# Kernel optimization log

Hardware: AMD Instinct MI355X
Metric: run time of the kernel (lower is better)

## Reference

```python
import jax, jax.numpy as jnp
import numpy as np

N_NODES = 100000
N_EDGES = 600000
D_IN = 128
D_HID = 128
N_CLASSES = 64


def setup_inputs() -> dict:
    key = jax.random.key(0)
    ks = jax.random.split(key, 8)
    x = jax.random.normal(ks[0], (N_NODES, D_IN), dtype=jnp.float32)
    src = jax.random.randint(ks[1], (N_EDGES,), 0, N_NODES, dtype=jnp.int32)
    dst = jax.random.randint(ks[2], (N_EDGES,), 0, N_NODES, dtype=jnp.int32)
    s = 1.0 / np.sqrt(D_IN)
    W_self1 = jax.random.normal(ks[3], (D_IN, D_HID), dtype=jnp.float32) * s
    W_neigh1 = jax.random.normal(ks[4], (D_IN, D_HID), dtype=jnp.float32) * s
    b1 = jnp.zeros((D_HID,), dtype=jnp.float32)
    s2 = 1.0 / np.sqrt(D_HID)
    W_self2 = jax.random.normal(ks[5], (D_HID, N_CLASSES), dtype=jnp.float32) * s2
    W_neigh2 = jax.random.normal(ks[6], (D_HID, N_CLASSES), dtype=jnp.float32) * s2
    b2 = jnp.zeros((N_CLASSES,), dtype=jnp.float32)
    return {"x": x, "src": src, "dst": dst,
            "W_self1": W_self1, "W_neigh1": W_neigh1, "b1": b1,
            "W_self2": W_self2, "W_neigh2": W_neigh2, "b2": b2}


def _sage_conv(h, src, dst, W_self, W_neigh, b):
    # mean aggregation over in-neighbors (DGL SAGEConv 'mean')
    n = h.shape[0]
    nbr_sum = jax.ops.segment_sum(h[src], dst, num_segments=n)  # [N, d]
    deg = jax.ops.segment_sum(jnp.ones(src.shape, h.dtype), dst, num_segments=n)
    nbr_mean = nbr_sum / jnp.maximum(deg, 1.0)[:, None]
    return h @ W_self + nbr_mean @ W_neigh + b


def reference(x, src, dst, W_self1, W_neigh1, b1, W_self2, W_neigh2, b2):
    # dropout is identity in eval mode
    h = _sage_conv(x, src, dst, W_self1, W_neigh1, b1)
    h = jax.nn.relu(h)
    h = _sage_conv(h, src, dst, W_self2, W_neigh2, b2)
    return h
```

## Files before the change

### kernel.cpp

```cpp
#include <hip/hip_runtime.h>

#define N_NODES 100000
#define N_EDGES 600000
#define K_DIM 128
#define M2 64
#define NT_TILES ((N_NODES + 63) / 64)
#define GEMM_GRID 256

#define NBKT 800
#define NPB 125
#define HIST_BLOCKS 64
#define EPB (N_EDGES / HIST_BLOCKS)
#define BSTRIDE 1024

using frag_ab = __attribute__((ext_vector_type(8))) short;
using frag_cd = __attribute__((ext_vector_type(4))) float;

__device__ __forceinline__ unsigned short f2b(float f) {
  unsigned u = __builtin_bit_cast(unsigned, f);
  u = (u + 0x7fffu + ((u >> 16) & 1u)) >> 16;
  return (unsigned short)u;
}

__device__ __forceinline__ void gload_lds16(const void* gsrc, void* ldst) {
  __builtin_amdgcn_global_load_lds(
      (const __attribute__((address_space(1))) void*)gsrc,
      (__attribute__((address_space(3))) void*)ldst, 16, 0, 0);
}

__device__ __forceinline__ void lgkm_barrier() {
  __builtin_amdgcn_sched_barrier(0);
  asm volatile("s_waitcnt lgkmcnt(0)" ::: "memory");
  __builtin_amdgcn_s_barrier();
  __builtin_amdgcn_sched_barrier(0);
}

#define XB_BLOCKS ((N_NODES * K_DIM / 4 + 255) / 256)
#define W_ELEMS ((128 + 128 + 64 + 64) * 128)
#define WB_BLOCKS ((W_ELEMS + 255) / 256)
__global__ __launch_bounds__(256) void conv_all(const float* __restrict__ x,
                                                unsigned short* __restrict__ xb,
                                                const float* __restrict__ Ws1,
                                                const float* __restrict__ Wn1,
                                                const float* __restrict__ Ws2,
                                                const float* __restrict__ Wn2,
                                                unsigned short* __restrict__ Ws1T,
                                                unsigned short* __restrict__ Wn1T,
                                                unsigned short* __restrict__ Ws2T,
                                                unsigned short* __restrict__ Wn2T,
                                                const int* __restrict__ src,
                                                const int* __restrict__ dst,
                                                int* __restrict__ gbucket,
                                                int* __restrict__ ebuf) {
  __shared__ int lcnt[NBKT];
  __shared__ int lbase[NBKT];
  if (blockIdx.x < HIST_BLOCKS) {
    int tid = threadIdx.x;
    for (int i = tid; i < NBKT; i += 256) lcnt[i] = 0;
    __syncthreads();
    int e0 = blockIdx.x * EPB;
    for (int e = e0 + tid; e < e0 + EPB; e += 256)
      atomicAdd(&lcnt[dst[e] / NPB], 1);
    __syncthreads();
    for (int i = tid; i < NBKT; i += 256) {
      int c = lcnt[i];
      lbase[i] = c ? atomicAdd(&gbucket[i], c) : 0;
      lcnt[i] = 0;
    }
    __syncthreads();
    for (int e = e0 + tid; e < e0 + EPB; e += 256) {
      int d = dst[e];
      int b = d / NPB;
      int p = lbase[b] + atomicAdd(&lcnt[b], 1);
      ebuf[b * BSTRIDE + p] = src[e] | ((d - b * NPB) << 20);
    }
  } else if (blockIdx.x < HIST_BLOCKS + XB_BLOCKS) {
    long i = (long)(blockIdx.x - HIST_BLOCKS) * 256 + threadIdx.x;
    if (i >= (long)N_NODES * K_DIM / 4) return;
    float4 v = *(const float4*)(x + i * 4);
    ushort4 o;
    o.x = f2b(v.x); o.y = f2b(v.y); o.z = f2b(v.z); o.w = f2b(v.w);
    *(ushort4*)(xb + i * 4) = o;
  } else {
    int i = (blockIdx.x - HIST_BLOCKS - XB_BLOCKS) * 256 + threadIdx.x;
    if (i >= W_ELEMS) return;
    const float* W;
    unsigned short* WT;
    int M, li;
    if (i < 128 * 128)               { W = Ws1; WT = Ws1T; M = 128; li = i; }
    else if (i < 2 * 128 * 128)      { W = Wn1; WT = Wn1T; M = 128; li = i - 128 * 128; }
    else if (i < 2 * 128 * 128 + 64 * 128) { W = Ws2; WT = Ws2T; M = 64; li = i - 2 * 128 * 128; }
    else                             { W = Wn2; WT = Wn2T; M = 64; li = i - 2 * 128 * 128 - 64 * 128; }
    int n = li >> 7, k = li & 127;
    WT[li] = f2b(W[k * M + n]);
  }
}

__global__ __launch_bounds__(512) void bucket_csr_agg1(const unsigned short* __restrict__ xb,
                                                       const int* __restrict__ ebuf,
                                                       const int* __restrict__ gbucket,
                                                       int* __restrict__ rp,
                                                       int* __restrict__ csr_src,
                                                       unsigned short* __restrict__ aggb) {
  __shared__ int cnt[128];
  __shared__ int sedge[BSTRIDE];
  int tid = threadIdx.x, b = blockIdx.x;
  int bs = b * BSTRIDE;
  int ecnt = gbucket[b];
  for (int i = tid; i < 128; i += 512) cnt[i] = 0;
  __syncthreads();

  int ln[2], lp[2], sv[2];
#pragma unroll
  for (int j = 0; j < 2; ++j) {
    int p = tid + j * 512;
    if (p < ecnt) {
      int pk = ebuf[bs + p];
      sv[j] = pk & 0xFFFFF;
      ln[j] = pk >> 20;
      lp[j] = atomicAdd(&cnt[ln[j]], 1);
    }
  }
  __syncthreads();
  for (int off = 1; off < 128; off <<= 1) {
    int t = 0;
    if (tid < 128 && tid >= off) t = cnt[tid - off];
    __syncthreads();
    if (tid < 128) cnt[tid] += t;
    __syncthreads();
  }
  for (int i = tid; i < 126; i += 512)
    rp[b * 126 + i] = bs + (i ? cnt[i - 1] : 0);
#pragma unroll
  for (int j = 0; j < 2; ++j) {
    int p = tid + j * 512;
    if (p < ecnt) {
      int l = ln[j];
      int loc = (l ? cnt[l - 1] : 0) + lp[j];
      sedge[loc] = sv[j];
      csr_src[bs + loc] = sv[j];
    }
  }
  __syncthreads();

  int nl = tid >> 4;
  int c = (tid & 15) << 3;
  for (int n0 = 0; n0 < NPB; n0 += 32) {
    int node = n0 + nl;
    if (node < NPB) {
      int beg = node ? cnt[node - 1] : 0;
      int end = cnt[node];
      float acc[8];
#pragma unroll
      for (int j = 0; j < 8; ++j) acc[j] = 0.f;
      for (int e0 = beg; e0 < end; e0 += 8) {
        int idx[8];
#pragma unroll
        for (int p = 0; p < 8; ++p) idx[p] = sedge[min(e0 + p, end - 1)];
        uint4 v[8];
#pragma unroll
        for (int p = 0; p < 8; ++p) v[p] = *(const uint4*)(xb + (size_t)idx[p] * K_DIM + c);
#pragma unroll
        for (int p = 0; p < 8; ++p) {
          float m = (e0 + p < end) ? 1.f : 0.f;
          unsigned u[4] = {v[p].x, v[p].y, v[p].z, v[p].w};
#pragma unroll
          for (int j = 0; j < 4; ++j) {
            acc[2 * j]     += m * __builtin_bit_cast(float, u[j] << 16);
            acc[2 * j + 1] += m * __builtin_bit_cast(float, u[j] & 0xffff0000u);
          }
        }
      }
      float inv = 1.0f / (float)max(end - beg, 1);
      uint4 o;
      unsigned* op = (unsigned*)&o;
#pragma unroll
      for (int j = 0; j < 4; ++j) {
        unsigned lo = f2b(acc[2 * j] * inv);
        unsigned hi = f2b(acc[2 * j + 1] * inv);
        op[j] = lo | (hi << 16);
      }
      *(uint4*)(aggb + (size_t)(b * NPB + node) * K_DIM + c) = o;
    }
  }
}

__global__ __launch_bounds__(256) void aggregate64_add(const unsigned short* __restrict__ g,
                                                       const int* __restrict__ rp,
                                                       const int* __restrict__ csr_src,
                                                       float* __restrict__ out, int n) {
  int t = blockIdx.x * blockDim.x + threadIdx.x;
  int node = t >> 3;
  int c = (t & 7) << 3;
  if (node >= n) return;
  int b = node / NPB;
  int i = node - b * NPB;
  int beg = rp[b * 126 + i], end = rp[b * 126 + i + 1];
  float acc[8];
#pragma unroll
  for (int j = 0; j < 8; ++j) acc[j] = 0.f;

  if (end > beg) {
    for (int e0 = beg; e0 < end; e0 += 8) {
      int idx[8];
#pragma unroll
      for (int p = 0; p < 8; ++p) idx[p] = csr_src[min(e0 + p, end - 1)];
      uint4 v[8];
#pragma unroll
      for (int p = 0; p < 8; ++p) v[p] = *(const uint4*)(g + (size_t)idx[p] * M2 + c);
#pragma unroll
      for (int p = 0; p < 8; ++p) {
        float m = (e0 + p < end) ? 1.f : 0.f;
        unsigned u[4] = {v[p].x, v[p].y, v[p].z, v[p].w};
#pragma unroll
        for (int j = 0; j < 4; ++j) {
          acc[2 * j]     += m * __builtin_bit_cast(float, u[j] << 16);
          acc[2 * j + 1] += m * __builtin_bit_cast(float, u[j] & 0xffff0000u);
        }
      }
    }
  }
  float inv = 1.0f / (float)max(end - beg, 1);
  float* op = out + (size_t)node * M2 + c;
  float4 o0 = *(float4*)(op);
  float4 o1 = *(float4*)(op + 4);
  o0.x += acc[0] * inv; o0.y += acc[1] * inv; o0.z += acc[2] * inv; o0.w += acc[3] * inv;
  o1.x += acc[4] * inv; o1.y += acc[5] * inv; o1.z += acc[6] * inv; o1.w += acc[7] * inv;
  *(float4*)(op) = o0;
  *(float4*)(op + 4) = o1;
}

__device__ __forceinline__ void stage_tile(const unsigned short* xb, const unsigned short* aggb,
                                           int t, char* dstbase, int tid, int wave, int N) {
#pragma unroll
  for (int it = 0; it < 2; ++it) {
    int L = it * 8192 + tid * 16;
    int row = L >> 8;
    int srb = (L & 255) ^ ((row & 7) << 4);
    int node = t * 64 + row;
    if (node >= N) node = N - 1;
    char* d = dstbase + it * 8192 + wave * 1024;
    gload_lds16((const char*)xb + (size_t)node * 256 + srb, d);
    gload_lds16((const char*)aggb + (size_t)node * 256 + srb, d + 16384);
  }
}

__global__ __launch_bounds__(512, 2) void sage_fused_gemm(const unsigned short* __restrict__ xb,
                                                          const unsigned short* __restrict__ aggb,
                                                          const unsigned short* __restrict__ Ws1T,
                                                          const unsigned short* __restrict__ Wn1T,
                                                          const float* __restrict__ b1,
                                                          const unsigned short* __restrict__ Ws2T,
                                                          const unsigned short* __restrict__ Wn2T,
                                                          const float* __restrict__ b2,
                                                          float* __restrict__ out,
                                                          unsigned short* __restrict__ g, int N) {
  __shared__ char sL[163840];

  const int tid = threadIdx.x;
  const int wave = tid >> 6;
  const int lane = tid & 63;
  const int l15 = lane & 15;
  const int q = lane >> 4;
  const int nodeq = wave >> 1;
  const int fhalf = wave & 1;
  const int fbase = fhalf * 64;

#pragma unroll
  for (int it = 0; it < 4; ++it) {
    int L = it * 8192 + tid * 16;
    int row = L >> 8;
    int srb = (L & 255) ^ ((row & 7) << 4);
    char* d = sL + it * 8192 + wave * 1024;
    gload_lds16((const char*)Ws1T + row * 256 + srb, d);
    gload_lds16((const char*)Wn1T + row * 256 + srb, d + 32768);
  }
#pragma unroll
  for (int it = 0; it < 2; ++it) {
    int L = it * 8192 + tid * 16;
    int row = L >> 8;
    int srb = (L & 255) ^ ((row & 7) << 4);
    char* d = sL + 65536 + it * 8192 + wave * 1024;
    gload_lds16((const char*)Ws2T + row * 256 + srb, d);
    gload_lds16((const char*)Wn2T + row * 256 + srb, d + 16384);
  }
  int tt = blockIdx.x;
  if (tt < NT_TILES) stage_tile(xb, aggb, tt, sL + 98304, tid, wave, N);

  float4 bv1[4], bv2[4];
#pragma unroll
  for (int ft = 0; ft < 4; ++ft) {
    bv1[ft] = *(const float4*)(b1 + fbase + ft * 16 + q * 4);
    bv2[ft] = *(const float4*)(b2 + ft * 16 + q * 4);
  }

  int li = 0;
  for (; tt < NT_TILES; tt += GEMM_GRID, ++li) {
    char* cur = sL + 98304 + (li & 1) * 32768;
    char* nxt = sL + 98304 + ((li + 1) & 1) * 32768;

    __syncthreads();

    if (tt + GEMM_GRID < NT_TILES)
      stage_tile(xb, aggb, tt + GEMM_GRID, nxt, tid, wave, N);

    frag_cd acc[4];
#pragma unroll
    for (int ft = 0; ft < 4; ++ft) acc[ft] = (frag_cd)(0.f);

    const int xrow = nodeq * 16 + l15;
    const int xswz = (xrow & 7) << 4;
#pragma unroll
    for (int kb = 0; kb < 4; ++kb) {
      int base = kb * 64 + q * 16;
      frag_ab axk = *(const frag_ab*)(cur + xrow * 256 + (base ^ xswz));
      frag_ab agk = *(const frag_ab*)(cur + 16384 + xrow * 256 + (base ^ xswz));
      frag_ab fs[4], fn[4];
#pragma unroll
      for (int ft = 0; ft < 4; ++ft) {
        int wrow = fbase + ft * 16 + l15;
        int woff = base ^ ((wrow & 7) << 4);
        fs[ft] = *(const frag_ab*)(sL + wrow * 256 + woff);
        fn[ft] = *(const frag_ab*)(sL + 32768 + wrow * 256 + woff);
      }
#pragma unroll
      for (int ft = 0; ft < 4; ++ft) {
        acc[ft] = __builtin_amdgcn_mfma_f32_16x16x32_bf16(fs[ft], axk, acc[ft], 0, 0, 0);
        acc[ft] = __builtin_amdgcn_mfma_f32_16x16x32_bf16(fn[ft], agk, acc[ft], 0, 0, 0);
      }
    }

    lgkm_barrier();

#pragma unroll
    for (int ft = 0; ft < 4; ++ft) {
      int f0 = fbase + ft * 16 + q * 4;
      ushort4 o;
      o.x = f2b(fmaxf(acc[ft][0] + bv1[ft].x, 0.f));
      o.y = f2b(fmaxf(acc[ft][1] + bv1[ft].y, 0.f));
      o.z = f2b(fmaxf(acc[ft][2] + bv1[ft].z, 0.f));
      o.w = f2b(fmaxf(acc[ft][3] + bv1[ft].w, 0.f));
      *(ushort4*)(cur + xrow * 256 + ((f0 * 2) ^ xswz)) = o;
    }

    lgkm_barrier();

    const char* w2b = sL + 65536 + fhalf * 16384;
    frag_cd acc2[4];
#pragma unroll
    for (int ft = 0; ft < 4; ++ft) acc2[ft] = (frag_cd)(0.f);

#pragma unroll
    for (int kb = 0; kb < 4; ++kb) {
      int base = kb * 64 + q * 16;
      frag_ab ah = *(const frag_ab*)(cur + xrow * 256 + (base ^ xswz));
      frag_ab w2[4];
#pragma unroll
      for (int ft = 0; ft < 4; ++ft) {
        int wr = ft * 16 + l15;
        w2[ft] = *(const frag_ab*)(w2b + wr * 256 + (base ^ ((wr & 7) << 4)));
      }
#pragma unroll
      for (int ft = 0; ft < 4; ++ft)
        acc2[ft] = __builtin_amdgcn_mfma_f32_16x16x32_bf16(w2[ft], ah, acc2[ft], 0, 0, 0);
    }

    int node = tt * 64 + nodeq * 16 + l15;
    if (node < N) {
      if (fhalf == 0) {
#pragma unroll
        for (int ft = 0; ft < 4; ++ft) {
          int f0 = ft * 16 + q * 4;
          float4 o;
          o.x = acc2[ft][0] + bv2[ft].x;
          o.y = acc2[ft][1] + bv2[ft].y;
          o.z = acc2[ft][2] + bv2[ft].z;
          o.w = acc2[ft][3] + bv2[ft].w;
          *(float4*)(out + (size_t)node * M2 + f0) = o;
        }
      } else {
#pragma unroll
        for (int ft = 0; ft < 4; ++ft) {
          int f0 = ft * 16 + q * 4;
          ushort4 o;
          o.x = f2b(acc2[ft][0]);
          o.y = f2b(acc2[ft][1]);
          o.z = f2b(acc2[ft][2]);
          o.w = f2b(acc2[ft][3]);
          *(ushort4*)(g + (size_t)node * M2 + f0) = o;
        }
      }
    }
  }
}

extern "C" void kernel_launch(void* const* d_in, const int* in_sizes, int n_in,
                              void* d_out, int out_size, void* d_ws, size_t ws_size,
                              hipStream_t stream) {
  const float* x   = (const float*)d_in[0];
  const int*   src = (const int*)d_in[1];
  const int*   dst = (const int*)d_in[2];
  const float* Ws1 = (const float*)d_in[3];
  const float* Wn1 = (const float*)d_in[4];
  const float* b1  = (const float*)d_in[5];
  const float* Ws2 = (const float*)d_in[6];
  const float* Wn2 = (const float*)d_in[7];
  const float* b2  = (const float*)d_in[8];
  float* out = (float*)d_out;

  char* ws = (char*)d_ws;
  size_t off = 0;
  auto alloc = [&](size_t bytes) {
    void* p = ws + off;
    off = (off + bytes + 4095) & ~(size_t)4095;
    return p;
  };
  int* gbucket  = (int*)alloc((size_t)NBKT * 4);
  int* ebuf     = (int*)alloc((size_t)NBKT * BSTRIDE * 4);
  int* rp       = (int*)alloc((size_t)NBKT * 126 * 4);
  int* csr_src  = (int*)alloc((size_t)NBKT * BSTRIDE * 4);
  unsigned short* xb   = (unsigned short*)alloc((size_t)N_NODES * K_DIM * 2);
  unsigned short* aggb = (unsigned short*)alloc((size_t)N_NODES * K_DIM * 2);
  unsigned short* g    = (unsigned short*)alloc((size_t)N_NODES * M2 * 2);
  unsigned short* Ws1T = (unsigned short*)alloc((size_t)128 * 128 * 2);
  unsigned short* Wn1T = (unsigned short*)alloc((size_t)128 * 128 * 2);
  unsigned short* Ws2T = (unsigned short*)alloc((size_t)64 * 128 * 2);
  unsigned short* Wn2T = (unsigned short*)alloc((size_t)64 * 128 * 2);

  hipMemsetAsync(gbucket, 0, (size_t)NBKT * 4, stream);

  conv_all<<<HIST_BLOCKS + XB_BLOCKS + WB_BLOCKS, 256, 0, stream>>>(
      x, xb, Ws1, Wn1, Ws2, Wn2, Ws1T, Wn1T, Ws2T, Wn2T, src, dst, gbucket, ebuf);

  bucket_csr_agg1<<<NBKT, 512, 0, stream>>>(xb, ebuf, gbucket, rp, csr_src, aggb);

  sage_fused_gemm<<<GEMM_GRID, 512, 0, stream>>>(
      xb, aggb, Ws1T, Wn1T, b1, Ws2T, Wn2T, b2, out, g, N_NODES);

  {
    long t = (long)N_NODES * 8;
    aggregate64_add<<<(int)((t + 255) / 256), 256, 0, stream>>>(g, rp, csr_src, out, N_NODES);
  }
}
```

Baseline: 213.0 us.

## Split edge bucket scatter into a separate wide kernel with precomputed positions

After: 203.2 us. -4.6%, faster.

```diff
diff --git a/kernel.cpp b/kernel.cpp
--- a/kernel.cpp
+++ b/kernel.cpp
@@ -35,7 +35,7 @@
   __builtin_amdgcn_sched_barrier(0);
 }
 
-#define XB_BLOCKS ((N_NODES * K_DIM / 4 + 255) / 256)
+#define XB_BLOCKS ((N_NODES * K_DIM / 8 + 255) / 256)
 #define W_ELEMS ((128 + 128 + 64 + 64) * 128)
 #define WB_BLOCKS ((W_ELEMS + 255) / 256)
 __global__ __launch_bounds__(256) void conv_all(const float* __restrict__ x,
@@ -48,39 +48,39 @@
                                                 unsigned short* __restrict__ Wn1T,
                                                 unsigned short* __restrict__ Ws2T,
                                                 unsigned short* __restrict__ Wn2T,
-                                                const int* __restrict__ src,
                                                 const int* __restrict__ dst,
+                                                int* __restrict__ pos,
                                                 int* __restrict__ gbucket,
-                                                int* __restrict__ ebuf) {
+                                                int* __restrict__ base_tbl) {
   __shared__ int lcnt[NBKT];
-  __shared__ int lbase[NBKT];
   if (blockIdx.x < HIST_BLOCKS) {
     int tid = threadIdx.x;
     for (int i = tid; i < NBKT; i += 256) lcnt[i] = 0;
     __syncthreads();
     int e0 = blockIdx.x * EPB;
-    for (int e = e0 + tid; e < e0 + EPB; e += 256)
-      atomicAdd(&lcnt[dst[e] / NPB], 1);
+    for (int e = e0 + tid; e < e0 + EPB; e += 256) {
+      int b = dst[e] / NPB;
+      pos[e] = atomicAdd(&lcnt[b], 1);
+    }
     __syncthreads();
     for (int i = tid; i < NBKT; i += 256) {
       int c = lcnt[i];
-      lbase[i] = c ? atomicAdd(&gbucket[i], c) : 0;
-      lcnt[i] = 0;
-    }
-    __syncthreads();
-    for (int e = e0 + tid; e < e0 + EPB; e += 256) {
-      int d = dst[e];
-      int b = d / NPB;
-      int p = lbase[b] + atomicAdd(&lcnt[b], 1);
-      ebuf[b * BSTRIDE + p] = src[e] | ((d - b * NPB) << 20);
+      if (c) base_tbl[blockIdx.x * NBKT + i] = atomicAdd(&gbucket[i], c);
     }
   } else if (blockIdx.x < HIST_BLOCKS + XB_BLOCKS) {
-    long i = (long)(blockIdx.x - HIST_BLOCKS) * 256 + threadIdx.x;
+    long t = (long)(blockIdx.x - HIST_BLOCKS) * 256 + threadIdx.x;
+    long i = t * 2;
     if (i >= (long)N_NODES * K_DIM / 4) return;
-    float4 v = *(const float4*)(x + i * 4);
-    ushort4 o;
-    o.x = f2b(v.x); o.y = f2b(v.y); o.z = f2b(v.z); o.w = f2b(v.w);
-    *(ushort4*)(xb + i * 4) = o;
+    float4 v0 = *(const float4*)(x + i * 4);
+    float4 v1 = *(const float4*)(x + i * 4 + 4);
+    ushort4 o0, o1;
+    o0.x = f2b(v0.x); o0.y = f2b(v0.y); o0.z = f2b(v0.z); o0.w = f2b(v0.w);
+    o1.x = f2b(v1.x); o1.y = f2b(v1.y); o1.z = f2b(v1.z); o1.w = f2b(v1.w);
+    *(uint4*)(xb + i * 4) = uint4{
+        (unsigned)o0.x | ((unsigned)o0.y << 16),
+        (unsigned)o0.z | ((unsigned)o0.w << 16),
+        (unsigned)o1.x | ((unsigned)o1.y << 16),
+        (unsigned)o1.z | ((unsigned)o1.w << 16)};
   } else {
     int i = (blockIdx.x - HIST_BLOCKS - XB_BLOCKS) * 256 + threadIdx.x;
     if (i >= W_ELEMS) return;
@@ -94,6 +94,19 @@
     int n = li >> 7, k = li & 127;
     WT[li] = f2b(W[k * M + n]);
   }
+}
+
+__global__ __launch_bounds__(256) void bucket_scatter(const int* __restrict__ src,
+                                                      const int* __restrict__ dst,
+                                                      const int* __restrict__ pos,
+                                                      const int* __restrict__ base_tbl,
+                                                      int* __restrict__ ebuf) {
+  int e = blockIdx.x * 256 + threadIdx.x;
+  if (e >= N_EDGES) return;
+  int d = dst[e];
+  int b = d / NPB;
+  int p = base_tbl[(e / EPB) * NBKT + b] + pos[e];
+  ebuf[b * BSTRIDE + p] = src[e] | ((d - b * NPB) << 20);
 }
 
 __global__ __launch_bounds__(512) void bucket_csr_agg1(const unsigned short* __restrict__ xb,
@@ -415,7 +428,9 @@
     off = (off + bytes + 4095) & ~(size_t)4095;
     return p;
   };
+  int* pos      = (int*)alloc((size_t)N_EDGES * 4);
   int* gbucket  = (int*)alloc((size_t)NBKT * 4);
+  int* base_tbl = (int*)alloc((size_t)HIST_BLOCKS * NBKT * 4);
   int* ebuf     = (int*)alloc((size_t)NBKT * BSTRIDE * 4);
   int* rp       = (int*)alloc((size_t)NBKT * 126 * 4);
   int* csr_src  = (int*)alloc((size_t)NBKT * BSTRIDE * 4);
@@ -430,7 +445,10 @@
   hipMemsetAsync(gbucket, 0, (size_t)NBKT * 4, stream);
 
   conv_all<<<HIST_BLOCKS + XB_BLOCKS + WB_BLOCKS, 256, 0, stream>>>(
-      x, xb, Ws1, Wn1, Ws2, Wn2, Ws1T, Wn1T, Ws2T, Wn2T, src, dst, gbucket, ebuf);
+      x, xb, Ws1, Wn1, Ws2, Wn2, Ws1T, Wn1T, Ws2T, Wn2T, dst, pos, gbucket, base_tbl);
+
+  bucket_scatter<<<(N_EDGES + 255) / 256, 256, 0, stream>>>(
+      src, dst, pos, base_tbl, ebuf);
 
   bucket_csr_agg1<<<NBKT, 512, 0, stream>>>(xb, ebuf, gbucket, rp, csr_src, aggb);
 
```
